# Performance work log

Hardware: AMD Instinct MI355X
Metric: run time of the kernel (lower is better)

## Reference

```python
import jax, jax.numpy as jnp
import numpy as np
from jax import lax

RANK = 8
ALPHA = 16.0
SCALING = ALPHA / RANK  # 2.0
C_IN, C_OUT, KH, KW = 128, 256, 3, 3


def setup_inputs() -> dict:
    key = jax.random.key(0)
    k1, k2, k3, k4, k5 = jax.random.split(key, 5)
    x = jax.random.normal(k1, (16, C_IN, 64, 64), dtype=jnp.float32)
    W = jax.random.normal(k2, (C_OUT, C_IN, KH, KW), dtype=jnp.float32) * 0.05
    b = jax.random.normal(k3, (C_OUT,), dtype=jnp.float32) * 0.05
    lora_A = jax.random.normal(k4, (RANK, C_IN * KH * KW), dtype=jnp.float32) * 0.02
    lora_B = jax.random.normal(k5, (C_OUT, RANK), dtype=jnp.float32) * 0.02
    return {"x": x, "W": W, "b": b, "lora_A": lora_A, "lora_B": lora_B}


def _conv(x, w, stride=(1, 1), padding=((1, 1), (1, 1))):
    return lax.conv_general_dilated(
        x, w, window_strides=stride, padding=padding,
        dimension_numbers=("NCHW", "OIHW", "NCHW"))


def reference(x, W, b, lora_A, lora_B):
    # Base (frozen) conv: [B, C_out, H, W]
    base_out = _conv(x, W) + b[None, :, None, None]
    # LoRA path. The torch code does im2col -> (BL, C_in*kh*kw) @ A.T @ B.T.
    # Because unfold flattens patches channel-major as (C_in, kh, kw), the
    # identical math is: rank-r conv with A reshaped as [rank, C_in, kh, kw],
    # then a 1x1 mix with B. Same result, no im2col materialization.
    A_k = lora_A.reshape(RANK, C_IN, KH, KW)
    h = _conv(x, A_k)                                   # [B, rank, H, W]
    lora_out = jnp.einsum("brhw,or->bohw", h, lora_B) * SCALING
    return base_out + lora_out
```

## Files before the change

### kernel.cpp

```cpp
#include <hip/hip_runtime.h>
#include <hip/hip_bf16.h>


#define CIN   128
#define COUT  256
#define NBAT  16
#define HPAD  66
#define WPAD  66

typedef __bf16 bf16x8 __attribute__((ext_vector_type(8)));
typedef float f32x4 __attribute__((ext_vector_type(4)));

#define XPAD_ELEMS ((size_t)NBAT * HPAD * WPAD * CIN)
#define XPAD_BYTES (XPAD_ELEMS * 2)
#define WT_ELEMS   ((size_t)9 * COUT * CIN)
#define WS_NEED    (XPAD_BYTES + WT_ELEMS * 2)

typedef __attribute__((address_space(1))) void gvoid;
typedef __attribute__((address_space(3))) void lvoid;

__device__ __forceinline__ void load_lds16(const void* g, void* l) {
    __builtin_amdgcn_global_load_lds((gvoid*)g, (lvoid*)l, 16, 0, 0);
}

__global__ void pad_prep(const float* __restrict__ x, __bf16* __restrict__ xpad,
                         const float* __restrict__ W, const float* __restrict__ lA,
                         const float* __restrict__ lB, __hip_bfloat16* __restrict__ Wt) {
    __shared__ float tile[128][66];
    const int t = threadIdx.x;

    if (blockIdx.x >= 1024) {
        const int idx = (blockIdx.x - 1024) * 256 + t;
        const int c = idx & 127;
        const int o = idx >> 7;
        float lb[8];
#pragma unroll
        for (int r = 0; r < 8; ++r) lb[r] = lB[o * 8 + r];
#pragma unroll
        for (int tap = 0; tap < 9; ++tap) {
            float acc = W[(o * 128 + c) * 9 + tap];
            float s = 0.f;
#pragma unroll
            for (int r = 0; r < 8; ++r)
                s += lb[r] * lA[r * 1152 + c * 9 + tap];
            Wt[tap * 32768 + idx] = __float2bfloat16(acc + 2.0f * s);
        }
        return;
    }

    const int n = blockIdx.x >> 6;
    const int h = blockIdx.x & 63;
    const float* src = x + (size_t)n * 128 * 4096 + (size_t)h * 64;
#pragma unroll
    for (int i = 0; i < 8; ++i) {
        int g  = i * 256 + t;
        int c  = g >> 4;
        int w4 = (g & 15) * 4;
        const float4 v = *reinterpret_cast<const float4*>(src + (size_t)c * 4096 + w4);
        const int wb = w4 ^ (((c >> 3) & 7) << 2);
        tile[c][wb + 0] = v.x; tile[c][wb + 1] = v.y;
        tile[c][wb + 2] = v.z; tile[c][wb + 3] = v.w;
    }
    __syncthreads();
    __bf16* dst = xpad + ((size_t)(n * 66 + h + 1) * 66 + 1) * 128;
#pragma unroll
    for (int i = 0; i < 4; ++i) {
        int g  = i * 256 + t;
        int w  = g >> 4;
        int c0 = (g & 15) * 8;
        const int swr = ((c0 >> 3) & 7) << 2;
        bf16x8 v;
#pragma unroll
        for (int j = 0; j < 8; ++j) v[j] = (__bf16)tile[c0 + j][w ^ swr];
        *reinterpret_cast<bf16x8*>(dst + (size_t)w * 128 + c0) = v;
    }
    bf16x8 z = {};
    __bf16* rowbase = xpad + (size_t)(n * 66 + h + 1) * 66 * 128;
    if (t < 32) {
        int ww = (t < 16) ? 0 : 65;
        int c0 = (t & 15) * 8;
        *reinterpret_cast<bf16x8*>(rowbase + (size_t)ww * 128 + c0) = z;
    }
    if (h == 0 || h == 63) {
        __bf16* hrow = xpad + (size_t)(n * 66 + (h == 0 ? 0 : 65)) * 66 * 128;
        for (int i = t; i < 66 * 16; i += 256)
            *reinterpret_cast<bf16x8*>(hrow + (size_t)i * 8) = z;
    }
}

__global__ void __launch_bounds__(512, 2) conv_mfma(
    const __bf16* __restrict__ xpad, const __bf16* __restrict__ Wt,
    const float* __restrict__ bias, float* __restrict__ out) {
    __shared__ __align__(16) __bf16 lds[65536];

    const int tid  = threadIdx.x;
    const int wv   = tid >> 6;
    const int lane = tid & 63;

    const int n  = blockIdx.x >> 4;
    const int h0 = (blockIdx.x & 15) << 2;

    const int lrow = lane >> 2;
    const int lswz = (((lane & 3) ^ ((lane >> 3) & 3)) << 3);
    const __bf16* aG[2];
    const __bf16* bG[2];
#pragma unroll
    for (int j = 0; j < 2; ++j) {
        const int r0 = j * 128 + wv * 16;
        aG[j] = Wt + (r0 + lrow) * 128 + lswz;
        bG[j] = xpad + (((size_t)(n * 66 + h0 + (r0 >> 6)) * 66 + (r0 & 63) + lrow) * 128) + lswz;
    }

    const int wo   = (wv >> 2) << 7;
    const int wpix = (wv & 3) << 6;
    const int fr   = lane & 15;
    const int fphys = (((lane >> 4) ^ ((lane >> 1) & 3)) << 3);
    const int a_rd = (wo + fr) * 32 + fphys;
    const int b_rd = (wpix + fr) * 32 + fphys;

    f32x4 acc[4][8] = {};

#define STAGE(u) do {                                                          \
        const int tap_ = (u) >> 2, cb_ = (u) & 3;                              \
        const int kh_ = (tap_ >= 6) ? 2 : (tap_ >= 3 ? 1 : 0);                 \
        const int kw_ = tap_ - kh_ * 3;                                        \
        const int ao_ = tap_ * 32768 + cb_ * 32;                               \
        const int bo_ = (kh_ * 66 + kw_) * 128 + cb_ * 32;                     \
        const int lb_ = ((u) & 3) * 8192;                                      \
        load_lds16(aG[0] + ao_, lds + lb_ + (wv * 16) * 32);                   \
        load_lds16(aG[1] + ao_, lds + lb_ + (128 + wv * 16) * 32);             \
        load_lds16(bG[0] + bo_, lds + 32768 + lb_ + (wv * 16) * 32);           \
        load_lds16(bG[1] + bo_, lds + 32768 + lb_ + (128 + wv * 16) * 32);     \
    } while (0)

#define COMPUTE(t) do {                                                        \
        const int lb_ = ((t) & 3) * 8192;                                      \
        const __bf16* Ab = lds + lb_ + a_rd;                                   \
        const __bf16* Bb = lds + 32768 + lb_ + b_rd;                           \
        bf16x8 af[8], bfr[4];                                                  \
        _Pragma("unroll")                                                      \
        for (int pi = 0; pi < 4; ++pi)                                         \
            bfr[pi] = *reinterpret_cast<const bf16x8*>(Bb + pi * 512);         \
        _Pragma("unroll")                                                      \
        for (int oi = 0; oi < 8; ++oi)                                         \
            af[oi] = *reinterpret_cast<const bf16x8*>(Ab + oi * 512);          \
        __builtin_amdgcn_s_setprio(1);                                         \
        _Pragma("unroll")                                                      \
        for (int pi = 0; pi < 4; ++pi)                                         \
            _Pragma("unroll")                                                  \
            for (int oi = 0; oi < 8; ++oi)                                     \
                acc[pi][oi] = __builtin_amdgcn_mfma_f32_16x16x32_bf16(         \
                    bfr[pi], af[oi], acc[pi][oi], 0, 0, 0);                    \
        __builtin_amdgcn_s_setprio(0);                                         \
    } while (0)

    STAGE(0); STAGE(1); STAGE(2);

    for (int t = 0; t < 33; ++t) {
        asm volatile("s_waitcnt vmcnt(8)" ::: "memory");
        __builtin_amdgcn_sched_barrier(0);
        __builtin_amdgcn_s_barrier();
        __builtin_amdgcn_sched_barrier(0);
        STAGE(t + 3);
        COMPUTE(t);
    }
    asm volatile("s_waitcnt vmcnt(8)" ::: "memory");
    __builtin_amdgcn_sched_barrier(0);
    __builtin_amdgcn_s_barrier();
    COMPUTE(33);
    asm volatile("s_waitcnt vmcnt(4)" ::: "memory");
    __builtin_amdgcn_sched_barrier(0);
    __builtin_amdgcn_s_barrier();
    COMPUTE(34);
    asm volatile("s_waitcnt vmcnt(0)" ::: "memory");
    __builtin_amdgcn_sched_barrier(0);
    __builtin_amdgcn_s_barrier();
    COMPUTE(35);

#undef STAGE
#undef COMPUTE

    const int col = lane & 15;
    const int q4  = (lane >> 4) << 2;
    const int h   = h0 + (wpix >> 6);
    float bo[8];
#pragma unroll
    for (int oi = 0; oi < 8; ++oi) bo[oi] = bias[wo + oi * 16 + col];
#pragma unroll
    for (int pi = 0; pi < 4; ++pi) {
        const int w0 = pi * 16 + q4;
#pragma unroll
        for (int oi = 0; oi < 8; ++oi) {
            const int o = wo + oi * 16 + col;
            f32x4 v;
#pragma unroll
            for (int j = 0; j < 4; ++j) v[j] = acc[pi][oi][j] + bo[oi];
            *reinterpret_cast<f32x4*>(out + (((size_t)n * 256 + o) * 64 + h) * 64 + w0) = v;
        }
    }
}

__global__ void conv_naive(const float* __restrict__ x, const float* __restrict__ W,
                           const float* __restrict__ b, const float* __restrict__ lA,
                           const float* __restrict__ lB, float* __restrict__ out) {
    int idx = blockIdx.x * 256 + threadIdx.x;
    int w = idx & 63, h = (idx >> 6) & 63, o = (idx >> 12) & 255, n = idx >> 20;
    float acc = b[o];
    float hr[8] = {0, 0, 0, 0, 0, 0, 0, 0};
    for (int c = 0; c < 128; ++c)
        for (int kh = 0; kh < 3; ++kh) {
            int hy = h + kh - 1;
            if (hy < 0 || hy > 63) continue;
            for (int kw = 0; kw < 3; ++kw) {
                int wx = w + kw - 1;
                if (wx < 0 || wx > 63) continue;
                float xv = x[((n * 128 + c) * 64 + hy) * 64 + wx];
                int ka = c * 9 + kh * 3 + kw;
                acc += W[(o * 128 + c) * 9 + kh * 3 + kw] * xv;
#pragma unroll
                for (int r = 0; r < 8; ++r) hr[r] += lA[r * 1152 + ka] * xv;
            }
        }
    float ls = 0.f;
#pragma unroll
    for (int r = 0; r < 8; ++r) ls += lB[o * 8 + r] * hr[r];
    out[idx] = acc + 2.0f * ls;
}

extern "C" void kernel_launch(void* const* d_in, const int* in_sizes, int n_in,
                              void* d_out, int out_size, void* d_ws, size_t ws_size,
                              hipStream_t stream) {
    const float* x  = (const float*)d_in[0];
    const float* W  = (const float*)d_in[1];
    const float* b  = (const float*)d_in[2];
    const float* lA = (const float*)d_in[3];
    const float* lB = (const float*)d_in[4];
    float* out = (float*)d_out;

    if (ws_size < WS_NEED) {
        conv_naive<<<out_size / 256, 256, 0, stream>>>(x, W, b, lA, lB, out);
        return;
    }

    __bf16* xpad = (__bf16*)d_ws;
    __hip_bfloat16* Wt = (__hip_bfloat16*)((char*)d_ws + XPAD_BYTES);

    pad_prep<<<1024 + 128, 256, 0, stream>>>(x, xpad, W, lA, lB, Wt);
    conv_mfma<<<256, 512, 0, stream>>>(xpad, (const __bf16*)Wt, b, out);
}
```

Measured before the change: 137.0 us.

## Load weight fragments directly into registers, bypassing LDS for A operand

Weights are pre-permuted in the prep kernel into MFMA fragment order so each wave can load its A fragments straight from global memory into registers with dwordx4 loads, double-buffered across iterations. LDS now holds only the input tiles, which halves shared memory per block and removes the LDS reads for weights. The pipeline depth for input staging drops from three stages ahead to two. The cost is more VGPRs for the two register weight buffers and per-wave redundant global weight traffic, since waves sharing output channels each fetch the same data, which relies on cache hits.

```diff
diff --git a/kernel.cpp b/kernel.cpp
--- a/kernel.cpp
+++ b/kernel.cpp
@@ -33,6 +33,12 @@
         const int idx = (blockIdx.x - 1024) * 256 + t;
         const int c = idx & 127;
         const int o = idx >> 7;
+        const int fr    = o & 15;
+        const int otile = o >> 4;
+        const int cb    = c >> 5;
+        const int kc    = (c >> 3) & 3;
+        const int j     = c & 7;
+        const int lane  = kc * 16 + fr;
         float lb[8];
 #pragma unroll
         for (int r = 0; r < 8; ++r) lb[r] = lB[o * 8 + r];
@@ -43,7 +49,8 @@
 #pragma unroll
             for (int r = 0; r < 8; ++r)
                 s += lb[r] * lA[r * 1152 + c * 9 + tap];
-            Wt[tap * 32768 + idx] = __float2bfloat16(acc + 2.0f * s);
+            const size_t widx = (((size_t)(tap * 4 + cb) * 16 + otile) * 64 + lane) * 8 + j;
+            Wt[widx] = __float2bfloat16(acc + 2.0f * s);
         }
         return;
     }
@@ -91,7 +98,7 @@
 __global__ void __launch_bounds__(512, 2) conv_mfma(
     const __bf16* __restrict__ xpad, const __bf16* __restrict__ Wt,
     const float* __restrict__ bias, float* __restrict__ out) {
-    __shared__ __align__(16) __bf16 lds[65536];
+    __shared__ __align__(16) __bf16 lds[32768];
 
     const int tid  = threadIdx.x;
     const int wv   = tid >> 6;
@@ -102,83 +109,106 @@
 
     const int lrow = lane >> 2;
     const int lswz = (((lane & 3) ^ ((lane >> 3) & 3)) << 3);
-    const __bf16* aG[2];
     const __bf16* bG[2];
 #pragma unroll
     for (int j = 0; j < 2; ++j) {
         const int r0 = j * 128 + wv * 16;
-        aG[j] = Wt + (r0 + lrow) * 128 + lswz;
         bG[j] = xpad + (((size_t)(n * 66 + h0 + (r0 >> 6)) * 66 + (r0 & 63) + lrow) * 128) + lswz;
     }
 
     const int wo   = (wv >> 2) << 7;
+    const int wot  = (wv >> 2) << 3;
     const int wpix = (wv & 3) << 6;
     const int fr   = lane & 15;
     const int fphys = (((lane >> 4) ^ ((lane >> 1) & 3)) << 3);
-    const int a_rd = (wo + fr) * 32 + fphys;
     const int b_rd = (wpix + fr) * 32 + fphys;
 
+    const __bf16* wG = Wt + (size_t)wot * 512 + lane * 8;
+
     f32x4 acc[4][8] = {};
+    f32x4 wA[8], wB[8];
+
+#define WL(dst, ptr, imm)                                                      \
+    asm volatile("global_load_dwordx4 %0, %1, off offset:" #imm                \
+                 : "=&v"(dst) : "v"(ptr) : "memory")
+
+#define WLOADS(WN, u) do {                                                     \
+        const __bf16* wp0_ = wG + (size_t)(u) * 8192;                          \
+        const __bf16* wp1_ = wp0_ + 2048;                                      \
+        WL(WN[0], wp0_, 0);    WL(WN[1], wp0_, 1024);                          \
+        WL(WN[2], wp0_, 2048); WL(WN[3], wp0_, 3072);                          \
+        WL(WN[4], wp1_, 0);    WL(WN[5], wp1_, 1024);                          \
+        WL(WN[6], wp1_, 2048); WL(WN[7], wp1_, 3072);                          \
+    } while (0)
 
 #define STAGE(u) do {                                                          \
-        const int tap_ = (u) >> 2, cb_ = (u) & 3;                              \
+        const int u_ = (u);                                                    \
+        const int tap_ = u_ >> 2, cb_ = u_ & 3;                                \
         const int kh_ = (tap_ >= 6) ? 2 : (tap_ >= 3 ? 1 : 0);                 \
         const int kw_ = tap_ - kh_ * 3;                                        \
-        const int ao_ = tap_ * 32768 + cb_ * 32;                               \
         const int bo_ = (kh_ * 66 + kw_) * 128 + cb_ * 32;                     \
-        const int lb_ = ((u) & 3) * 8192;                                      \
-        load_lds16(aG[0] + ao_, lds + lb_ + (wv * 16) * 32);                   \
-        load_lds16(aG[1] + ao_, lds + lb_ + (128 + wv * 16) * 32);             \
-        load_lds16(bG[0] + bo_, lds + 32768 + lb_ + (wv * 16) * 32);           \
-        load_lds16(bG[1] + bo_, lds + 32768 + lb_ + (128 + wv * 16) * 32);     \
-    } while (0)
-
-#define COMPUTE(t) do {                                                        \
-        const int lb_ = ((t) & 3) * 8192;                                      \
-        const __bf16* Ab = lds + lb_ + a_rd;                                   \
-        const __bf16* Bb = lds + 32768 + lb_ + b_rd;                           \
-        bf16x8 af[8], bfr[4];                                                  \
+        const int lb_ = (u_ & 3) * 8192;                                       \
+        load_lds16(bG[0] + bo_, lds + lb_ + (wv * 16) * 32);                   \
+        load_lds16(bG[1] + bo_, lds + lb_ + (128 + wv * 16) * 32);             \
+    } while (0)
+
+#define COMPUTE(t_, WC) do {                                                   \
+        const __bf16* Bb = lds + ((t_) & 3) * 8192 + b_rd;                     \
+        bf16x8 bfr[4];                                                         \
         _Pragma("unroll")                                                      \
         for (int pi = 0; pi < 4; ++pi)                                         \
             bfr[pi] = *reinterpret_cast<const bf16x8*>(Bb + pi * 512);         \
-        _Pragma("unroll")                                                      \
-        for (int oi = 0; oi < 8; ++oi)                                         \
-            af[oi] = *reinterpret_cast<const bf16x8*>(Ab + oi * 512);          \
         __builtin_amdgcn_s_setprio(1);                                         \
         _Pragma("unroll")                                                      \
         for (int pi = 0; pi < 4; ++pi)                                         \
             _Pragma("unroll")                                                  \
             for (int oi = 0; oi < 8; ++oi)                                     \
                 acc[pi][oi] = __builtin_amdgcn_mfma_f32_16x16x32_bf16(         \
-                    bfr[pi], af[oi], acc[pi][oi], 0, 0, 0);                    \
+                    bfr[pi], __builtin_bit_cast(bf16x8, WC[oi]),               \
+                    acc[pi][oi], 0, 0, 0);                                     \
         __builtin_amdgcn_s_setprio(0);                                         \
     } while (0)
 
-    STAGE(0); STAGE(1); STAGE(2);
-
-    for (int t = 0; t < 33; ++t) {
-        asm volatile("s_waitcnt vmcnt(8)" ::: "memory");
-        __builtin_amdgcn_sched_barrier(0);
-        __builtin_amdgcn_s_barrier();
-        __builtin_amdgcn_sched_barrier(0);
-        STAGE(t + 3);
-        COMPUTE(t);
-    }
-    asm volatile("s_waitcnt vmcnt(8)" ::: "memory");
+#define BODY(t_, WC, WN) do {                                                  \
+        asm volatile("s_waitcnt vmcnt(2)" ::: "memory");                       \
+        __builtin_amdgcn_sched_barrier(0);                                     \
+        __builtin_amdgcn_s_barrier();                                          \
+        __builtin_amdgcn_sched_barrier(0);                                     \
+        WLOADS(WN, (t_) + 1);                                                  \
+        __builtin_amdgcn_sched_barrier(0);                                     \
+        STAGE((t_) + 2);                                                       \
+        __builtin_amdgcn_sched_barrier(0);                                     \
+        COMPUTE(t_, WC);                                                       \
+    } while (0)
+
+    WLOADS(wA, 0);
+    __builtin_amdgcn_sched_barrier(0);
+    STAGE(0);
+    STAGE(1);
+    __builtin_amdgcn_sched_barrier(0);
+
+    for (int tt = 0; tt < 17; ++tt) {
+        BODY(2 * tt,     wA, wB);
+        BODY(2 * tt + 1, wB, wA);
+    }
+    asm volatile("s_waitcnt vmcnt(2)" ::: "memory");
     __builtin_amdgcn_sched_barrier(0);
     __builtin_amdgcn_s_barrier();
-    COMPUTE(33);
-    asm volatile("s_waitcnt vmcnt(4)" ::: "memory");
+    __builtin_amdgcn_sched_barrier(0);
+    WLOADS(wB, 35);
+    __builtin_amdgcn_sched_barrier(0);
+    COMPUTE(34, wA);
+    asm volatile("s_waitcnt vmcnt(0)" ::: "memory");
     __builtin_amdgcn_sched_barrier(0);
     __builtin_amdgcn_s_barrier();
-    COMPUTE(34);
-    asm volatile("s_waitcnt vmcnt(0)" ::: "memory");
-    __builtin_amdgcn_sched_barrier(0);
-    __builtin_amdgcn_s_barrier();
-    COMPUTE(35);
-
+    __builtin_amdgcn_sched_barrier(0);
+    COMPUTE(35, wB);
+
+#undef BODY
+#undef COMPUTE
 #undef STAGE
-#undef COMPUTE
+#undef WLOADS
+#undef WL
 
     const int col = lane & 15;
     const int q4  = (lane >> 4) << 2;
```

Result: no change. 136.3 us (-0.5%).
